# Kernel optimization log

Measured on AMD Instinct MI355X. Metric: run time of the kernel, lower is better.

The kernel has to match this reference:

```python
import jax, jax.numpy as jnp
import numpy as np

B, T, V, D = 16, 200, 25, 128
N_Q, N_E = 4, 1024
BETA, ALPHA, SLOPE, LN_EPS = 0.25, 0.1, 0.2, 1e-5

def _ring_adjacency(v):
    A = np.zeros((v, v), dtype=np.float32)
    for i in range(v):
        A[i, (i + 1) % v] = 1.0
        A[i, (i - 1) % v] = 1.0
    A = A + np.eye(v, dtype=np.float32)  # A + I, as in module
    d_inv_sqrt = 1.0 / np.sqrt(A.sum(1))
    return (d_inv_sqrt[:, None] * A) * d_inv_sqrt[None, :]

def setup_inputs() -> dict:
    key = jax.random.key(0)
    k_z, k_e, k_w = jax.random.split(key, 3)
    z = jax.random.normal(k_z, (B, T, V, D), dtype=jnp.float32)
    # xavier_uniform for each [n_e, e_dim] codebook
    lim = float(np.sqrt(6.0 / (N_E + D)))
    emb = jax.random.uniform(k_e, (N_Q, N_E, D), dtype=jnp.float32, minval=-lim, maxval=lim)
    wlim = float(np.sqrt(1.0 / D))
    gcn_w = jax.random.uniform(k_w, (D, D), dtype=jnp.float32, minval=-wlim, maxval=wlim)
    return {
        "z": z,
        "emb": emb,
        "A_norm": jnp.asarray(_ring_adjacency(V)),
        "gcn_w": gcn_w,
        "gcn_b": jnp.zeros((D,), jnp.float32),
        "ln_scale": jnp.ones((D,), jnp.float32),
        "ln_bias": jnp.zeros((D,), jnp.float32),
    }

def _gcn_refine(residual, A_norm, gcn_w, gcn_b, ln_scale, ln_bias):
    # residual: [N, V, d]
    neigh = jnp.einsum('vw,nwd->nvd', A_norm, residual)
    neigh = neigh @ gcn_w.T + gcn_b                      # nn.Linear
    neigh = jnp.where(neigh >= 0, neigh, SLOPE * neigh)  # LeakyReLU(0.2)
    mu = neigh.mean(-1, keepdims=True)
    var = ((neigh - mu) ** 2).mean(-1, keepdims=True)
    neigh = (neigh - mu) / jnp.sqrt(var + LN_EPS) * ln_scale + ln_bias
    return residual + ALPHA * neigh

def reference(z, emb, A_norm, gcn_w, gcn_b, ln_scale, ln_bias):
    b, t, v, d = z.shape
    n_q = emb.shape[0]
    zf = z.reshape(b * t, v, d)
    residual = zf
    cum = jnp.zeros_like(zf)
    losses, idxs = [], []
    for k in range(n_q):
        refined = _gcn_refine(residual, A_norm, gcn_w, gcn_b, ln_scale, ln_bias)
        W = emb[k]                               # [n_e, d]
        flat = refined.reshape(-1, d)            # [N*V, d]
        dist = ((flat ** 2).sum(1, keepdims=True)
                - 2.0 * flat @ W.T
                + (W ** 2).sum(1)[None, :])
        idx = jnp.argmin(dist, axis=1)           # [N*V]
        q = W[idx].reshape(b * t, v, d)          # == one_hot @ W
        # commit and codebook terms are identical squared errors -> (1+beta)*mse
        diff = q - jax.lax.stop_gradient(residual)
        losses.append((1.0 + BETA) * (diff ** 2).mean(-1))
        cum = cum + q
        residual = residual - q
        idxs.append(idx.reshape(b * t, v))
    zq = zf + jax.lax.stop_gradient(cum - zf)    # straight-through
    total_loss = jnp.stack(losses, 0).mean()
    indices = jnp.stack(idxs, -1).reshape(b, t, v, n_q)
    return zq.reshape(b, t, v, d), total_loss, indices
```

## Files before the change

### kernel.cpp

```cpp
#include <hip/hip_runtime.h>

#define ZQ_N    10240000
#define IDX_OFF 10240001
#define FLT_BIG 3.402823466e38f

typedef _Float16 f16x8 __attribute__((ext_vector_type(8)));
typedef float    f32x4 __attribute__((ext_vector_type(4)));

__global__ __launch_bounds__(256) void k_wsq(const float* __restrict__ emb,
                                             float* __restrict__ wsq,
                                             float* __restrict__ loss_part) {
    int t = threadIdx.x;
    int g = blockIdx.x * 256 + t;
    if (g < 1024) loss_part[g] = 0.f;
    int row = blockIdx.x * 64 + (t >> 2);
    int seg = t & 3;
    const float4* p = (const float4*)(emb + row * 128 + seg * 32);
    float a = 0.f;
#pragma unroll
    for (int i = 0; i < 8; i++) {
        float4 w = p[i];
        a = fmaf(w.x, w.x, a); a = fmaf(w.y, w.y, a);
        a = fmaf(w.z, w.z, a); a = fmaf(w.w, w.w, a);
    }
    a += __shfl_xor(a, 1);
    a += __shfl_xor(a, 2);
    if (seg == 0) wsq[row] = a;
}

__global__ __launch_bounds__(256) void k_wsplit(const float* __restrict__ emb,
        _Float16* __restrict__ wh, _Float16* __restrict__ wl,
        const float* __restrict__ gw,
        _Float16* __restrict__ gh, _Float16* __restrict__ gl) {
    int c = blockIdx.x * 256 + threadIdx.x;
    int q   = c >> 14;
    int col = (c >> 4) & 1023;
    int k8  = (c & 15) * 8;
    const float* srcp = emb + q * 131072 + col * 128 + k8;
    float4 a = *(const float4*)(srcp);
    float4 b = *(const float4*)(srcp + 4);
    float vv[8] = {a.x, a.y, a.z, a.w, b.x, b.y, b.z, b.w};
    union { _Float16 h[8]; uint4 u4; } ph, pl;
#pragma unroll
    for (int j = 0; j < 8; j++) {
        float v = vv[j] * 1024.f;
        _Float16 h = (_Float16)v;
        float r1 = v - (float)h;
        ph.h[j] = h; pl.h[j] = (_Float16)r1;
    }
    int p  = col >> 8, w = (col >> 6) & 3, ct = (col >> 4) & 3, lm = col & 15;
    int ks = k8 >> 5, quad = (k8 >> 3) & 3;
    int off = ((((p * 4 + w) * 4 + ks) * 4 + ct) * 512 + (quad * 16 + lm) * 8);
    *(uint4*)(wh + q * 131072 + off) = ph.u4;
    *(uint4*)(wl + q * 131072 + off) = pl.u4;

    if (c < 16384) {
        float v = gw[c] * 1024.f;
        _Float16 h = (_Float16)v;
        float r1 = v - (float)h;
        gh[c] = h; gl[c] = (_Float16)r1;
    }
}

__global__ __launch_bounds__(256) void k_refine(const float* __restrict__ src,
        float* __restrict__ refined, float* __restrict__ s_out,
        const float* __restrict__ An,
        const _Float16* __restrict__ gh, const _Float16* __restrict__ gl,
        const float* __restrict__ gb, const float* __restrict__ lsc,
        const float* __restrict__ lbi) {
    __shared__ __align__(16) float Rn[25 * 128];
    __shared__ __align__(16) unsigned char nbuf[2 * 32 * 136 * 2];
    __shared__ float Al[625];
    _Float16* nh = (_Float16*)nbuf;
    _Float16* nl = (_Float16*)(nbuf + 8704);
    float*    nei = (float*)nbuf;
    const int tid = threadIdx.x;
    const int n = blockIdx.x;

    const float4* sp = (const float4*)(src + n * 3200);
    float4* Rn4 = (float4*)Rn;
    for (int i = tid; i < 800; i += 256) Rn4[i] = sp[i];
    for (int i = tid; i < 625; i += 256) Al[i] = An[i];
    __syncthreads();

    for (int i = tid; i < 512; i += 256) {
        int r = i >> 4, k8 = (i & 15) * 8;
        union { _Float16 h[8]; uint4 u4; } ph, pl;
        if (r < 25) {
            int vm = (r == 0) ? 24 : r - 1;
            int vp = (r == 24) ? 0 : r + 1;
            float am = Al[r * 25 + vm], a0 = Al[r * 25 + r], ap = Al[r * 25 + vp];
#pragma unroll
            for (int j = 0; j < 8; j++) {
                int d = k8 + j;
                float val = am * Rn[vm * 128 + d];
                val = fmaf(a0, Rn[r  * 128 + d], val);
                val = fmaf(ap, Rn[vp * 128 + d], val);
                float v1 = val * 1024.f;
                _Float16 h = (_Float16)v1; float fh = (float)h;
                ph.h[j] = h; pl.h[j] = (_Float16)(v1 - fh);
            }
        } else {
            ph.u4 = make_uint4(0u, 0u, 0u, 0u);
            pl.u4 = make_uint4(0u, 0u, 0u, 0u);
        }
        int off = r * 136 + k8;
        *(uint4*)(&nh[off]) = ph.u4;
        *(uint4*)(&nl[off]) = pl.u4;
    }
    __syncthreads();

    {
        const int lane = tid & 63;
        const int wv   = tid >> 6;
        const int quad = lane >> 4;
        const int lm   = lane & 15;
        const int bbase = (wv * 32 + lm) * 128 + quad * 8;
        const int abase = lm * 136 + quad * 8;

        f32x4 racc[2][2];
#pragma unroll
        for (int a = 0; a < 2; a++)
#pragma unroll
            for (int b = 0; b < 2; b++) racc[a][b] = (f32x4){0.f, 0.f, 0.f, 0.f};

#pragma unroll
        for (int k0 = 0; k0 < 4; k0++) {
            const int ko = k0 * 32;
            f16x8 ah[2], al[2];
#pragma unroll
            for (int mt = 0; mt < 2; mt++) {
                ah[mt] = *(const f16x8*)(&nh[abase + mt * (16 * 136) + ko]);
                al[mt] = *(const f16x8*)(&nl[abase + mt * (16 * 136) + ko]);
            }
            f16x8 bh[2], bl[2];
#pragma unroll
            for (int ct = 0; ct < 2; ct++) {
                bh[ct] = *(const f16x8*)(gh + bbase + ct * (16 * 128) + ko);
                bl[ct] = *(const f16x8*)(gl + bbase + ct * (16 * 128) + ko);
            }
#pragma unroll
            for (int ct = 0; ct < 2; ct++)
#pragma unroll
                for (int mt = 0; mt < 2; mt++)
                    racc[ct][mt] = __builtin_amdgcn_mfma_f32_16x16x32_f16(ah[mt], bh[ct], racc[ct][mt], 0, 0, 0);
#pragma unroll
            for (int ct = 0; ct < 2; ct++)
#pragma unroll
                for (int mt = 0; mt < 2; mt++)
                    racc[ct][mt] = __builtin_amdgcn_mfma_f32_16x16x32_f16(ah[mt], bl[ct], racc[ct][mt], 0, 0, 0);
#pragma unroll
            for (int ct = 0; ct < 2; ct++)
#pragma unroll
                for (int mt = 0; mt < 2; mt++)
                    racc[ct][mt] = __builtin_amdgcn_mfma_f32_16x16x32_f16(al[mt], bh[ct], racc[ct][mt], 0, 0, 0);
        }

        __syncthreads();

#pragma unroll
        for (int ct = 0; ct < 2; ct++)
#pragma unroll
            for (int mt = 0; mt < 2; mt++)
#pragma unroll
                for (int rg = 0; rg < 4; rg++) {
                    int row = mt * 16 + quad * 4 + rg;
                    if (row < 25)
                        nei[row * 132 + wv * 32 + ct * 16 + lm] =
                            racc[ct][mt][rg] * 9.5367431640625e-07f;
                }
    }
    __syncthreads();

    const int dpg = tid & 31;
    const int vs  = tid >> 5;
    const int dp0 = dpg * 4;

    float4 b4  = *(const float4*)(gb + dp0);
    float4 sc4 = *(const float4*)(lsc + dp0);
    float4 bi4 = *(const float4*)(lbi + dp0);
    const float bb[4] = {b4.x, b4.y, b4.z, b4.w};
    const float sc[4] = {sc4.x, sc4.y, sc4.z, sc4.w};
    const float bi[4] = {bi4.x, bi4.y, bi4.z, bi4.w};

#pragma unroll
    for (int i = 0; i < 4; i++) {
        int v = vs + 8 * i;
        if (v >= 25) break;
        float4 y4 = *(const float4*)(&nei[v * 132 + dp0]);
        const float yin[4] = {y4.x, y4.y, y4.z, y4.w};
        float y[4];
#pragma unroll
        for (int c = 0; c < 4; c++) {
            float t = yin[c] + bb[c];
            y[c] = (t >= 0.f) ? t : 0.2f * t;
        }
        float s1 = y[0] + y[1] + y[2] + y[3];
#pragma unroll
        for (int m = 1; m <= 16; m <<= 1) s1 += __shfl_xor(s1, m);
        float mu = s1 * (1.f / 128.f);
        float d2 = 0.f;
#pragma unroll
        for (int c = 0; c < 4; c++) { float t = y[c] - mu; d2 = fmaf(t, t, d2); }
#pragma unroll
        for (int m = 1; m <= 16; m <<= 1) d2 += __shfl_xor(d2, m);
        float inv = 1.f / sqrtf(d2 * (1.f / 128.f) + 1e-5f);

        float4 rn4 = *(const float4*)(&Rn[v * 128 + dp0]);
        const float rn[4] = {rn4.x, rn4.y, rn4.z, rn4.w};
        float o[4];
#pragma unroll
        for (int c = 0; c < 4; c++)
            o[c] = rn[c] + 0.1f * ((y[c] - mu) * inv * sc[c] + bi[c]);

        *(float4*)(refined + (n * 25 + v) * 128 + dp0) =
            make_float4(o[0], o[1], o[2], o[3]);

        float ss = 0.f;
#pragma unroll
        for (int c = 0; c < 4; c++) ss = fmaf(o[c], o[c], ss);
#pragma unroll
        for (int m = 1; m <= 16; m <<= 1) ss += __shfl_xor(ss, m);
        if (dpg == 0) s_out[n * 25 + v] = ss;
    }
}


#define VQ_LOADB(BH, BL, IT) do {                                              \
    const int _o = ((((IT) >> 2) * 4 + w) * 16 + ((IT) & 3) * 4) * 512 + lane * 8; \
    BH[0] = *(const f16x8*)(wh + _o);        BL[0] = *(const f16x8*)(wl + _o);        \
    BH[1] = *(const f16x8*)(wh + _o + 512);  BL[1] = *(const f16x8*)(wl + _o + 512);  \
    BH[2] = *(const f16x8*)(wh + _o + 1024); BL[2] = *(const f16x8*)(wl + _o + 1024); \
    BH[3] = *(const f16x8*)(wh + _o + 1536); BL[3] = *(const f16x8*)(wl + _o + 1536); \
} while (0)

#define VQ_STEP(IT, BH, BL) do {                                               \
    const int _ko = abase + ((IT) & 3) * 32;                                   \
    f16x8 _ah[4], _al[4];                                                      \
    _Pragma("unroll")                                                          \
    for (int _rt = 0; _rt < 4; _rt++) {                                        \
        const int _off = _ko + _rt * (16 * 136);                               \
        _ah[_rt] = *(const f16x8*)(&xh_s[_off]);                               \
        _al[_rt] = *(const f16x8*)(&xl_s[_off]);                               \
    }                                                                          \
    _Pragma("unroll")                                                          \
    for (int _ct = 0; _ct < 4; _ct++)                                          \
        _Pragma("unroll")                                                      \
        for (int _rt = 0; _rt < 4; _rt++)                                      \
            acc[_ct][_rt] = __builtin_amdgcn_mfma_f32_16x16x32_f16(_ah[_rt], BH[_ct], acc[_ct][_rt], 0, 0, 0); \
    _Pragma("unroll")                                                          \
    for (int _ct = 0; _ct < 4; _ct++)                                          \
        _Pragma("unroll")                                                      \
        for (int _rt = 0; _rt < 4; _rt++)                                      \
            acc[_ct][_rt] = __builtin_amdgcn_mfma_f32_16x16x32_f16(_ah[_rt], BL[_ct], acc[_ct][_rt], 0, 0, 0); \
    _Pragma("unroll")                                                          \
    for (int _ct = 0; _ct < 4; _ct++)                                          \
        _Pragma("unroll")                                                      \
        for (int _rt = 0; _rt < 4; _rt++)                                      \
            acc[_ct][_rt] = __builtin_amdgcn_mfma_f32_16x16x32_f16(_al[_rt], BH[_ct], acc[_ct][_rt], 0, 0, 0); \
} while (0)

#define VQ_EPI(P) do {                                                         \
    float _sr[16];                                                             \
    _Pragma("unroll")                                                          \
    for (int _rt = 0; _rt < 4; _rt++) {                                        \
        float4 _t = *(const float4*)(s_g + row0 + _rt * 16 + quad * 4);        \
        _sr[_rt * 4 + 0] = _t.x; _sr[_rt * 4 + 1] = _t.y;                      \
        _sr[_rt * 4 + 2] = _t.z; _sr[_rt * 4 + 3] = _t.w;                      \
    }                                                                          \
    _Pragma("unroll")                                                          \
    for (int _ct = 0; _ct < 4; _ct++) {                                        \
        const int _col = (P) * 256 + w * 64 + _ct * 16 + lm;                   \
        const float _wq = wsq_k[_col];                                         \
        _Pragma("unroll")                                                      \
        for (int _rt = 0; _rt < 4; _rt++) {                                    \
            _Pragma("unroll")                                                  \
            for (int _rg = 0; _rg < 4; _rg++) {                                \
                float _d = (_sr[_rt * 4 + _rg]                                 \
                            - 1.9073486328125e-06f * acc[_ct][_rt][_rg]) + _wq;\
                int _s = _rt * 4 + _rg;                                        \
                if (_d < bestv[_s]) { bestv[_s] = _d; besti[_s] = _col; }      \
            }                                                                  \
        }                                                                      \
    }                                                                          \
} while (0)

__global__ __launch_bounds__(256) void k_vq(const float* __restrict__ refined,
        const _Float16* __restrict__ wh,
        const _Float16* __restrict__ wl,
        const float* __restrict__ emb_k, const float* __restrict__ wsq_k,
        const float* __restrict__ s_g,
        const float* res_src, float* res_dst,
        float* __restrict__ idx_out, int stage) {
    __shared__ __align__(16) _Float16 xh_s[64 * 136];
    __shared__ __align__(16) _Float16 xl_s[64 * 136];
    __shared__ int il[64];
    const int tid = threadIdx.x;
    const int row0 = blockIdx.x * 64;

    const int lane = tid & 63;
    const int w    = tid >> 6;
    const int quad = lane >> 4;
    const int lm   = lane & 15;

    const int abase = lm * 136 + quad * 8;

    f16x8 bha[4], bla[4], bhb[4], blb[4];
    VQ_LOADB(bha, bla, 0);

    for (int i = tid; i < 1024; i += 256) {
        int r = i >> 4, k8 = (i & 15) * 8;
        const float* srcp = refined + (row0 + r) * 128 + k8;
        float4 a = *(const float4*)(srcp);
        float4 b = *(const float4*)(srcp + 4);
        float vv[8] = {a.x, a.y, a.z, a.w, b.x, b.y, b.z, b.w};
        union { _Float16 h[8]; uint4 u4; } ph, pl;
#pragma unroll
        for (int j = 0; j < 8; j++) {
            float v = vv[j] * 1024.f;
            _Float16 h = (_Float16)v; float fh = (float)h;
            float r1 = v - fh;
            ph.h[j] = h; pl.h[j] = (_Float16)r1;
        }
        int off = r * 136 + k8;
        *(uint4*)(&xh_s[off]) = ph.u4;
        *(uint4*)(&xl_s[off]) = pl.u4;
    }
    __syncthreads();

    float bestv[16];
    int   besti[16];
#pragma unroll
    for (int s = 0; s < 16; s++) { bestv[s] = FLT_BIG; besti[s] = 0; }

    f32x4 acc[4][4];

#pragma unroll
    for (int ith = 0; ith < 8; ith++) {
        const int it0 = ith * 2, it1 = it0 + 1;
        VQ_LOADB(bhb, blb, it1);
        if ((it0 & 3) == 0) {
#pragma unroll
            for (int a = 0; a < 4; a++)
#pragma unroll
                for (int b = 0; b < 4; b++) acc[a][b] = (f32x4){0.f, 0.f, 0.f, 0.f};
        }
        VQ_STEP(it0, bha, bla);
        if (it1 < 15) VQ_LOADB(bha, bla, it1 + 1);
        VQ_STEP(it1, bhb, blb);
        if ((it1 & 3) == 3) VQ_EPI(it1 >> 2);
    }

#pragma unroll
    for (int s = 0; s < 16; s++) {
#pragma unroll
        for (int m = 1; m <= 8; m <<= 1) {
            float ov = __shfl_xor(bestv[s], m);
            int   oi = __shfl_xor(besti[s], m);
            if (ov < bestv[s] || (ov == bestv[s] && oi < besti[s])) {
                bestv[s] = ov; besti[s] = oi;
            }
        }
    }

    __syncthreads();
    float* redv = (float*)xh_s;
    int*   redi = (int*)xl_s;
    if (lm == 0) {
#pragma unroll
        for (int s = 0; s < 16; s++) {
            int row = (s >> 2) * 16 + quad * 4 + (s & 3);
            redv[w * 64 + row] = bestv[s];
            redi[w * 64 + row] = besti[s];
        }
    }
    __syncthreads();
    if (tid < 64) {
        float bv = redv[tid]; int bi = redi[tid];
#pragma unroll
        for (int ww = 1; ww < 4; ww++) {
            float v2 = redv[ww * 64 + tid]; int i2 = redi[ww * 64 + tid];
            if (v2 < bv || (v2 == bv && i2 < bi)) { bv = v2; bi = i2; }
        }
        il[tid] = bi;
        idx_out[(row0 + tid) * 4 + stage] = (float)bi;
    }
    __syncthreads();

    if (stage < 3) {
        const float4* rp = (const float4*)(res_src + row0 * 128);
        float4* rw = (float4*)(res_dst + row0 * 128);
#pragma unroll
        for (int j = 0; j < 8; j++) {
            int idx4 = tid + j * 256;
            int r    = idx4 >> 5;
            int c    = idx4 & 31;
            int code = il[r];
            float4 q4 = *(const float4*)(emb_k + code * 128 + c * 4);
            float4 r4 = rp[idx4];
            rw[idx4] = make_float4(r4.x - q4.x, r4.y - q4.y, r4.z - q4.z, r4.w - q4.w);
        }
    }
}

#define FIN_STAGE(K, ACC) do {                                                 \
    const float4 q = *(const float4*)(emb + (K) * 131072 + codes[r * 4 + (K)] * 128 + c4); \
    float dx = q.x - rv.x, dy = q.y - rv.y, dz = q.z - rv.z, dw = q.w - rv.w;  \
    ACC = fmaf(dx, dx, ACC); ACC = fmaf(dy, dy, ACC);                          \
    ACC = fmaf(dz, dz, ACC); ACC = fmaf(dw, dw, ACC);                          \
    s4.x += q.x; s4.y += q.y; s4.z += q.z; s4.w += q.w;                        \
    rv.x -= q.x; rv.y -= q.y; rv.z -= q.z; rv.w -= q.w;                        \
} while (0)

__global__ __launch_bounds__(256) void k_final(const float* __restrict__ z,
        const float* __restrict__ emb, const float* __restrict__ idx_f,
        float* __restrict__ zq, float* __restrict__ loss_part) {
    __shared__ int codes[256];
    const int tid = threadIdx.x;
    const int row0 = blockIdx.x * 64;
    codes[tid] = (int)idx_f[row0 * 4 + tid];
    __syncthreads();

    const float4* zp = (const float4*)(z + row0 * 128);
    float4* zqp = (float4*)(zq + row0 * 128);
    float a0 = 0.f, a1 = 0.f, a2 = 0.f, a3 = 0.f;
#pragma unroll
    for (int j = 0; j < 8; j++) {
        int idx4 = tid + j * 256;
        int r = idx4 >> 5;
        int c4 = (idx4 & 31) * 4;
        float4 rv = zp[idx4];
        float4 s4 = make_float4(0.f, 0.f, 0.f, 0.f);
        FIN_STAGE(0, a0);
        FIN_STAGE(1, a1);
        FIN_STAGE(2, a2);
        FIN_STAGE(3, a3);
        zqp[idx4] = s4;
    }
#pragma unroll
    for (int m = 1; m <= 32; m <<= 1) {
        a0 += __shfl_xor(a0, m); a1 += __shfl_xor(a1, m);
        a2 += __shfl_xor(a2, m); a3 += __shfl_xor(a3, m);
    }
    if ((tid & 63) == 0) {
        float* slot = &loss_part[blockIdx.x & 1023];
        atomicAdd(slot, a0); atomicAdd(slot, a1);
        atomicAdd(slot, a2); atomicAdd(slot, a3);
    }
}

__global__ __launch_bounds__(256) void k_loss(const float* __restrict__ loss_part,
                                              float* __restrict__ out) {
    int t = threadIdx.x;
    float a = loss_part[t] + loss_part[t + 256] + loss_part[t + 512] + loss_part[t + 768];
#pragma unroll
    for (int m = 1; m <= 32; m <<= 1) a += __shfl_xor(a, m);
    __shared__ float w[4];
    if ((t & 63) == 0) w[t >> 6] = a;
    __syncthreads();
    if (t == 0) {
        float s = w[0] + w[1] + w[2] + w[3];
        out[ZQ_N] = s * (1.25f / (128.f * 320000.f));
    }
}

extern "C" void kernel_launch(void* const* d_in, const int* in_sizes, int n_in,
                              void* d_out, int out_size, void* d_ws, size_t ws_size,
                              hipStream_t stream) {
    (void)in_sizes; (void)n_in; (void)out_size; (void)ws_size;
    const float* z   = (const float*)d_in[0];
    const float* emb = (const float*)d_in[1];
    const float* An  = (const float*)d_in[2];
    const float* gw  = (const float*)d_in[3];
    const float* gb  = (const float*)d_in[4];
    const float* lsc = (const float*)d_in[5];
    const float* lbi = (const float*)d_in[6];

    float* out     = (float*)d_out;
    float* zq      = out;
    float* idx_out = out + IDX_OFF;

    float* ws        = (float*)d_ws;
    float* resbuf    = ws;
    float* refined   = ws + 10240000;
    _Float16* gh_f16 = (_Float16*)(ws + 20480000);
    _Float16* gl_f16 = (_Float16*)(ws + 20488192);
    _Float16* wh_f16 = (_Float16*)(ws + 20496384);
    _Float16* wl_f16 = (_Float16*)(ws + 20758528);
    float* s_g       = ws + 21020672;
    float* wsq       = ws + 21100672;
    float* loss_part = ws + 21104768;

    k_wsq<<<64, 256, 0, stream>>>(emb, wsq, loss_part);
    k_wsplit<<<256, 256, 0, stream>>>(emb, wh_f16, wl_f16, gw, gh_f16, gl_f16);
    for (int k = 0; k < 4; k++) {
        const float* src = (k == 0) ? z : resbuf;
        k_refine<<<3200, 256, 0, stream>>>(src, refined, s_g, An,
                                           gh_f16, gl_f16, gb, lsc, lbi);
        k_vq<<<1250, 256, 0, stream>>>(refined,
                                       wh_f16 + k * 131072, wl_f16 + k * 131072,
                                       emb + k * 131072, wsq + k * 1024,
                                       s_g, src, resbuf, idx_out, k);
    }
    k_final<<<1250, 256, 0, stream>>>(z, emb, idx_out, zq, loss_part);
    k_loss<<<1, 256, 0, stream>>>(loss_part, out);
}
```

Before: 801.0 us.

## Recompute residual from z and codes in refine instead of storing residual buffer

Removes the residual write-back from the VQ kernel and the materialized residual buffer. The refine kernel now rebuilds each residual from z minus the codebook rows selected in earlier stages, using the stored indices. This trades one residual write and one residual read per stage for extra codebook gathers, which are small and likely cache-resident. The work is uneven across stages because later stages gather more rows.

```diff
diff --git a/kernel.cpp b/kernel.cpp
--- a/kernel.cpp
+++ b/kernel.cpp
@@ -62,7 +62,8 @@
     }
 }
 
-__global__ __launch_bounds__(256) void k_refine(const float* __restrict__ src,
+__global__ __launch_bounds__(256) void k_refine(const float* __restrict__ zbase,
+        const float* __restrict__ emb, const float* __restrict__ idx_f, int stage,
         float* __restrict__ refined, float* __restrict__ s_out,
         const float* __restrict__ An,
         const _Float16* __restrict__ gh, const _Float16* __restrict__ gl,
@@ -71,16 +72,34 @@
     __shared__ __align__(16) float Rn[25 * 128];
     __shared__ __align__(16) unsigned char nbuf[2 * 32 * 136 * 2];
     __shared__ float Al[625];
+    __shared__ int cds[75];
     _Float16* nh = (_Float16*)nbuf;
     _Float16* nl = (_Float16*)(nbuf + 8704);
     float*    nei = (float*)nbuf;
     const int tid = threadIdx.x;
     const int n = blockIdx.x;
 
-    const float4* sp = (const float4*)(src + n * 3200);
+    if (tid < 75) {
+        int r = tid / 3, j = tid - r * 3;
+        if (j < stage) cds[tid] = (int)idx_f[(n * 25 + r) * 4 + j];
+    }
+    for (int i = tid; i < 625; i += 256) Al[i] = An[i];
+    __syncthreads();
+
+    const float4* zp = (const float4*)(zbase + n * 3200);
     float4* Rn4 = (float4*)Rn;
-    for (int i = tid; i < 800; i += 256) Rn4[i] = sp[i];
-    for (int i = tid; i < 625; i += 256) Al[i] = An[i];
+    for (int i = tid; i < 800; i += 256) {
+        float4 rv = zp[i];
+        int r = i >> 5, c4 = (i & 31) * 4;
+#pragma unroll
+        for (int j = 0; j < 3; j++) {
+            if (j < stage) {
+                const float4 q = *(const float4*)(emb + j * 131072 + cds[r * 3 + j] * 128 + c4);
+                rv.x -= q.x; rv.y -= q.y; rv.z -= q.z; rv.w -= q.w;
+            }
+        }
+        Rn4[i] = rv;
+    }
     __syncthreads();
 
     for (int i = tid; i < 512; i += 256) {
@@ -288,13 +307,11 @@
 __global__ __launch_bounds__(256) void k_vq(const float* __restrict__ refined,
         const _Float16* __restrict__ wh,
         const _Float16* __restrict__ wl,
-        const float* __restrict__ emb_k, const float* __restrict__ wsq_k,
+        const float* __restrict__ wsq_k,
         const float* __restrict__ s_g,
-        const float* res_src, float* res_dst,
         float* __restrict__ idx_out, int stage) {
     __shared__ __align__(16) _Float16 xh_s[64 * 136];
     __shared__ __align__(16) _Float16 xl_s[64 * 136];
-    __shared__ int il[64];
     const int tid = threadIdx.x;
     const int row0 = blockIdx.x * 64;
 
@@ -382,24 +399,7 @@
             float v2 = redv[ww * 64 + tid]; int i2 = redi[ww * 64 + tid];
             if (v2 < bv || (v2 == bv && i2 < bi)) { bv = v2; bi = i2; }
         }
-        il[tid] = bi;
         idx_out[(row0 + tid) * 4 + stage] = (float)bi;
-    }
-    __syncthreads();
-
-    if (stage < 3) {
-        const float4* rp = (const float4*)(res_src + row0 * 128);
-        float4* rw = (float4*)(res_dst + row0 * 128);
-#pragma unroll
-        for (int j = 0; j < 8; j++) {
-            int idx4 = tid + j * 256;
-            int r    = idx4 >> 5;
-            int c    = idx4 & 31;
-            int code = il[r];
-            float4 q4 = *(const float4*)(emb_k + code * 128 + c * 4);
-            float4 r4 = rp[idx4];
-            rw[idx4] = make_float4(r4.x - q4.x, r4.y - q4.y, r4.z - q4.z, r4.w - q4.w);
-        }
     }
 }
 
@@ -481,7 +481,6 @@
     float* idx_out = out + IDX_OFF;
 
     float* ws        = (float*)d_ws;
-    float* resbuf    = ws;
     float* refined   = ws + 10240000;
     _Float16* gh_f16 = (_Float16*)(ws + 20480000);
     _Float16* gl_f16 = (_Float16*)(ws + 20488192);
@@ -494,13 +493,13 @@
     k_wsq<<<64, 256, 0, stream>>>(emb, wsq, loss_part);
     k_wsplit<<<256, 256, 0, stream>>>(emb, wh_f16, wl_f16, gw, gh_f16, gl_f16);
     for (int k = 0; k < 4; k++) {
-        const float* src = (k == 0) ? z : resbuf;
-        k_refine<<<3200, 256, 0, stream>>>(src, refined, s_g, An,
+        k_refine<<<3200, 256, 0, stream>>>(z, emb, idx_out, k,
+                                           refined, s_g, An,
                                            gh_f16, gl_f16, gb, lsc, lbi);
         k_vq<<<1250, 256, 0, stream>>>(refined,
                                        wh_f16 + k * 131072, wl_f16 + k * 131072,
-                                       emb + k * 131072, wsq + k * 1024,
-                                       s_g, src, resbuf, idx_out, k);
+                                       wsq + k * 1024,
+                                       s_g, idx_out, k);
     }
     k_final<<<1250, 256, 0, stream>>>(z, emb, idx_out, zq, loss_part);
     k_loss<<<1, 256, 0, stream>>>(loss_part, out);
```

New measurement: 761.5 us. 1.05x faster.
